# Kernel tuning notes

Hardware: AMD Instinct MI355X
Metric: run time of the kernel (lower is better)

## Reference

```python
import jax, jax.numpy as jnp
import numpy as np

B, T, C = 16, 1023, 2048
N_LAYER, LAYER_ID = 24, 12


def setup_inputs() -> dict:
    key = jax.random.key(0)
    k0, k1, k2, k3, k4 = jax.random.split(key, 5)
    x = jax.random.normal(k0, (B, T, C), jnp.float32)
    # decay schedule exactly as in RWKV_TimeMix.__init__ (first_sa_layer_id = 1)
    f1 = 3.0 + (LAYER_ID - 1) / (N_LAYER - 2) * (1.2 - 3.0)
    f2 = 0.65 + (LAYER_ID - 1) / (N_LAYER - 2) * (0.4 - 0.65)
    h = np.arange(C, dtype=np.float64)
    decay_speed = np.power(f2, h / (C - 1) * 7) * f1
    time_decay = jnp.asarray(np.log(decay_speed), jnp.float32)          # [C]
    time_first = jnp.full((C,), float(np.log(0.3)), jnp.float32)        # [C]
    time_mix = jnp.concatenate([jnp.zeros((C // 2,), jnp.float32),
                                jnp.ones((C - C // 2,), jnp.float32)])  # [C]
    s = 0.02
    Wk = jax.random.normal(k1, (C, C), jnp.float32) * s
    Wv = jax.random.normal(k2, (C, C), jnp.float32) * s
    Wr = jax.random.normal(k3, (C, C), jnp.float32) * s
    Wo = jax.random.normal(k4, (C, C), jnp.float32) * s
    z = jnp.zeros((B, C), jnp.float32)
    return {"x": x, "time_decay": time_decay, "time_first": time_first,
            "time_mix": time_mix, "Wk": Wk, "Wv": Wv, "Wr": Wr, "Wo": Wo,
            "xx": z, "aa": z, "bb": z, "mm": z}


def reference(x, time_decay, time_first, time_mix, Wk, Wv, Wr, Wo, xx, aa, bb, mm):
    Bn, Tn, Cn = x.shape
    # time_shift: prepend carried last-token state xx, drop last
    x_shift = jnp.concatenate([xx[:, None, :], x[:, :-1, :]], axis=1)
    xm = x * time_mix + x_shift * (1.0 - time_mix)
    k = xm @ Wk.T                       # [B, T, C]
    v = xm @ Wv.T
    r = xm @ Wr.T
    # running-max renorm to the nearest power of two: ldexp(0.5, frexp(max_t k).exponent)
    kmax = jax.lax.stop_gradient(jnp.max(k, axis=1))   # [B, C], max over time
    _, expo = jnp.frexp(kmax)
    mm_new = jnp.ldexp(jnp.float32(0.5), expo)          # [B, C]
    k = jnp.exp(k - mm_new[:, None, :])
    kv = k * v
    # TimeX kernel weights: w[c, T-1-delta] = exp(-exp(time_decay[c]) * (delta-1)) = d**(delta-1),
    # w[c, T-1] = exp(time_first[c]); so wk[t] = e_first*k[t] + sum_{u<t} d^{t-1-u} k[u] -> linear scan
    d = jnp.exp(-jnp.exp(time_decay))                   # [C] per-channel decay (= w[...,-3])
    e_first = jnp.exp(time_first)                       # [C] (w[...,-1])
    rsf = jnp.exp(mm - mm_new)                          # rescale carried state to new renorm
    k_seq = jnp.concatenate([(bb * rsf)[:, None, :], k], axis=1)    # [B, T+1, C]
    kv_seq = jnp.concatenate([(aa * rsf)[:, None, :], kv], axis=1)  # [B, T+1, C]

    def step(carry, inp):
        Sk, Skv = carry
        kt, kvt = inp
        out = (e_first * kt + Sk, e_first * kvt + Skv)
        return (d * Sk + kt, d * Skv + kvt), out

    init = (jnp.zeros((Bn, Cn), x.dtype), jnp.zeros((Bn, Cn), x.dtype))
    seq = (jnp.swapaxes(k_seq, 0, 1), jnp.swapaxes(kv_seq, 0, 1))   # [T+1, B, C]
    _, (wk_s, wkv_s) = jax.lax.scan(step, init, seq)
    wk = jnp.swapaxes(wk_s[1:], 0, 1)     # drop state slot -> [B, T, C]
    wkv = jnp.swapaxes(wkv_s[1:], 0, 1)
    rwkv = jax.nn.sigmoid(r) * jnp.nan_to_num(wkv / wk)
    return rwkv @ Wo.T
```

## Files before the change

### kernel.cpp

```cpp
#include <hip/hip_runtime.h>
#include <hip/hip_bf16.h>
#include <math.h>
#include <float.h>

#define BB 16
#define TT 1023
#define CC 2048
#define M_ROWS (BB * TT)
#define MP 16384
#define N3 (3 * CC)
#define NCH 16
#define CHL 64

typedef __attribute__((ext_vector_type(8))) short bfrag;
typedef __attribute__((ext_vector_type(4))) float f32x4;
typedef __attribute__((ext_vector_type(4))) short short4v;

__device__ __forceinline__ void async16(const void* g, void* l) {
  __builtin_amdgcn_global_load_lds((const __attribute__((address_space(1))) void*)g,
                                   (__attribute__((address_space(3))) void*)l, 16, 0, 0);
}

__device__ __forceinline__ short bfb(float f) {
  __hip_bfloat16 h = __float2bfloat16(f);
  return *reinterpret_cast<short*>(&h);
}

__global__ void cast_weights(const float* __restrict__ Wk, const float* __restrict__ Wv,
                             const float* __restrict__ Wr, const float* __restrict__ Wo,
                             __hip_bfloat16* __restrict__ W3, __hip_bfloat16* __restrict__ WoB) {
  size_t i4 = (size_t)blockIdx.x * 256 + threadIdx.x;
  size_t i = i4 * 4;
  float4 a = *(const float4*)(Wk + i);
  float4 b = *(const float4*)(Wv + i);
  float4 c = *(const float4*)(Wr + i);
  float4 d = *(const float4*)(Wo + i);
  *(short4v*)((short*)W3 + i)              = short4v{bfb(a.x), bfb(a.y), bfb(a.z), bfb(a.w)};
  *(short4v*)((short*)W3 + i + CC * CC)    = short4v{bfb(b.x), bfb(b.y), bfb(b.z), bfb(b.w)};
  *(short4v*)((short*)W3 + i + 2 * CC * CC) = short4v{bfb(c.x), bfb(c.y), bfb(c.z), bfb(c.w)};
  *(short4v*)((short*)WoB + i)             = short4v{bfb(d.x), bfb(d.y), bfb(d.z), bfb(d.w)};
}

__global__ void build_xm(const float* __restrict__ x, const float* __restrict__ xx,
                         const float* __restrict__ tmix, __hip_bfloat16* __restrict__ xm) {
  int m = blockIdx.x;
  short* orow = (short*)xm + (size_t)m * CC;
  if (m >= M_ROWS) {
    for (int c = threadIdx.x; c < CC / 4; c += 256)
      ((short4v*)orow)[c] = short4v{0, 0, 0, 0};
    return;
  }
  int b = m / TT, t = m - b * TT;
  const float* xrow = x + (size_t)m * CC;
  const float* xprev = (t == 0) ? (xx + (size_t)b * CC) : (xrow - CC);
  for (int c = threadIdx.x; c < CC / 4; c += 256) {
    float4 xv = ((const float4*)xrow)[c];
    float4 pv = ((const float4*)xprev)[c];
    float4 tm = ((const float4*)tmix)[c];
    ((short4v*)orow)[c] = short4v{
        bfb(xv.x * tm.x + pv.x * (1.0f - tm.x)),
        bfb(xv.y * tm.y + pv.y * (1.0f - tm.y)),
        bfb(xv.z * tm.z + pv.z * (1.0f - tm.z)),
        bfb(xv.w * tm.w + pv.w * (1.0f - tm.w))};
  }
}

template <int MODE>
__global__ __launch_bounds__(512, 2)
void gemm256(const short* __restrict__ A, const short* __restrict__ Bw,
             float* __restrict__ outF, __hip_bfloat16* __restrict__ outV,
             __hip_bfloat16* __restrict__ outR) {
  __shared__ short lds[65536];

  const int lane = threadIdx.x & 63, wid = threadIdx.x >> 6;
  const int wr = wid >> 2, wc = wid & 3;

  const int nx = gridDim.x;
  const int nwg = nx * gridDim.y;
  const int bid = blockIdx.y * nx + blockIdx.x;
  const int q = nwg >> 3;
  const int swz = (bid & 7) * q + (bid >> 3);
  const int mBase = (swz / nx) * 256;
  const int nBase = (swz % nx) * 256;

  const int srow = lane >> 2;
  const int scol = (((lane & 3) ^ ((lane >> 3) & 3)) * 8);
  const int stgOff = wid * 1024 + lane * 8;
  const short* aSrcBase = A  + (size_t)(mBase + wid * 32 + srow) * CC + scol;
  const short* bSrcBase = Bw + (size_t)(nBase + wid * 32 + srow) * CC + scol;

  const int ldOff = (lane & 15) * 32 + (((lane >> 4) ^ ((lane >> 1) & 3)) * 8);

  f32x4 acc[2][4][4] = {};
  bfrag bq[2][4];

#define RGNA(buf, kh) ((buf) * 32768 + (kh) * 8192)
#define RGNB(buf, kh) (16384 + (buf) * 32768 + (kh) * 8192)

#define STG_A(buf, kh, tk) do { \
    const short* _s = aSrcBase + ((tk) * 64 + (kh) * 32); \
    short* _d = lds + RGNA(buf, kh) + stgOff; \
    async16(_s, _d); async16(_s + (size_t)16 * CC, _d + 512); } while (0)

#define STG_B(buf, kh, tk) do { \
    const short* _s = bSrcBase + ((tk) * 64 + (kh) * 32); \
    short* _d = lds + RGNB(buf, kh) + stgOff; \
    async16(_s, _d); async16(_s + (size_t)16 * CC, _d + 512); } while (0)

#define STG4(buf, tk) do { \
    STG_A(buf, 0, tk); STG_B(buf, 0, tk); \
    STG_A(buf, 1, tk); STG_B(buf, 1, tk); } while (0)

#define VM0 asm volatile("s_waitcnt vmcnt(0)" ::: "memory")

#define PHA(buf, STAGE) do { \
    bfrag aq[2][4]; \
    _Pragma("unroll") \
    for (int kh = 0; kh < 2; ++kh) { \
      _Pragma("unroll") \
      for (int n = 0; n < 4; ++n) \
        bq[kh][n] = *(const bfrag*)(lds + RGNB(buf, kh) + (wc * 64 + n * 16) * 32 + ldOff); \
      _Pragma("unroll") \
      for (int f = 0; f < 4; ++f) \
        aq[kh][f] = *(const bfrag*)(lds + RGNA(buf, kh) + (wr * 128 + f * 16) * 32 + ldOff); \
    } \
    STAGE; \
    __builtin_amdgcn_s_barrier(); \
    __builtin_amdgcn_s_setprio(1); \
    _Pragma("unroll") \
    for (int kh = 0; kh < 2; ++kh) \
      _Pragma("unroll") \
      for (int f = 0; f < 4; ++f) \
        _Pragma("unroll") \
        for (int n = 0; n < 4; ++n) \
          acc[0][f][n] = __builtin_amdgcn_mfma_f32_16x16x32_bf16(aq[kh][f], bq[kh][n], acc[0][f][n], 0, 0, 0); \
    __builtin_amdgcn_s_setprio(0); \
    __builtin_amdgcn_s_barrier(); } while (0)

#define PHB(buf, WAIT) do { \
    bfrag aq[2][4]; \
    _Pragma("unroll") \
    for (int kh = 0; kh < 2; ++kh) \
      _Pragma("unroll") \
      for (int f = 0; f < 4; ++f) \
        aq[kh][f] = *(const bfrag*)(lds + RGNA(buf, kh) + (wr * 128 + 64 + f * 16) * 32 + ldOff); \
    __builtin_amdgcn_s_barrier(); \
    __builtin_amdgcn_s_setprio(1); \
    _Pragma("unroll") \
    for (int kh = 0; kh < 2; ++kh) \
      _Pragma("unroll") \
      for (int f = 0; f < 4; ++f) \
        _Pragma("unroll") \
        for (int n = 0; n < 4; ++n) \
          acc[1][f][n] = __builtin_amdgcn_mfma_f32_16x16x32_bf16(aq[kh][f], bq[kh][n], acc[1][f][n], 0, 0, 0); \
    __builtin_amdgcn_s_setprio(0); \
    WAIT; \
    __builtin_amdgcn_s_barrier(); } while (0)

  STG4(0, 0);
  VM0;
  __builtin_amdgcn_s_barrier();

  for (int ti = 0; ti < 30; ti += 2) {
    PHA(0, STG4(1, ti + 1));
    PHB(0, VM0);
    PHA(1, STG4(0, ti + 2));
    PHB(1, VM0);
  }
  PHA(0, STG4(1, 31));
  PHB(0, VM0);
  PHA(1, );
  PHB(1, );

#undef PHA
#undef PHB
#undef VM0
#undef STG4
#undef STG_A
#undef STG_B
#undef RGNA
#undef RGNB

#pragma unroll
  for (int mh = 0; mh < 2; ++mh)
#pragma unroll
    for (int f = 0; f < 4; ++f) {
      const int row0 = mBase + wr * 128 + mh * 64 + f * 16 + (lane >> 4) * 4;
      const int col0 = nBase + wc * 64 + (lane & 15);
#pragma unroll
      for (int n = 0; n < 4; ++n) {
        const int col = col0 + n * 16;
#pragma unroll
        for (int rr = 0; rr < 4; ++rr) {
          const int row = row0 + rr;
          if (row < M_ROWS) {
            float val = acc[mh][f][n][rr];
            if constexpr (MODE == 0) {
              outF[(size_t)row * CC + col] = val;
            } else {
              if (col < CC)          outF[(size_t)row * CC + col] = val;
              else if (col < 2 * CC) outV[(size_t)row * CC + (col - CC)] = __float2bfloat16(val);
              else                   outR[(size_t)row * CC + (col - 2 * CC)] = __float2bfloat16(val);
            }
          }
        }
      }
    }
}

__global__ __launch_bounds__(1024)
void scan_fuse2(const float* __restrict__ kraw, const __hip_bfloat16* __restrict__ v,
                const __hip_bfloat16* __restrict__ r, const float* __restrict__ aa,
                const float* __restrict__ bb, const float* __restrict__ mm,
                const float* __restrict__ tdec, const float* __restrict__ tfir,
                __hip_bfloat16* __restrict__ rwkv) {
  __shared__ float sBk[NCH][64], sBkv[NCH][64], sSk[NCH][64], sSkv[NCH][64];

  const int lane = threadIdx.x & 63, wid = threadIdx.x >> 6;
  const int c = blockIdx.x * 64 + lane;
  const int b = blockIdx.y;
  const int i = b * CC + c;

  const float dexp = expf(tdec[c]);
  const float d    = expf(-dexp);
  const float ef   = expf(tfir[c]);

  const int t0 = wid * CHL;
  const int t1 = (t0 + CHL < TT) ? t0 + CHL : TT;
  const size_t base = (size_t)b * TT * CC + c;

  if (wid < NCH - 1) {
    float Bk = 0.0f, Bkv = 0.0f;
    size_t off = base + (size_t)t0 * CC;
#pragma unroll 4
    for (int t = t0; t < t1; ++t, off += CC) {
      float kk = expf(kraw[off]);
      float kv = kk * __bfloat162float(v[off]);
      Bk = d * Bk + kk;
      Bkv = d * Bkv + kv;
    }
    sBk[wid][lane] = Bk;
    sBkv[wid][lane] = Bkv;
  }
  __syncthreads();

  if (wid == 0) {
    const float d64 = expf(-dexp * (float)CHL);
    const float sc = expf(mm[i]);
    float S = bb[i] * sc, Sv = aa[i] * sc;
#pragma unroll
    for (int j = 0; j < NCH; ++j) {
      sSk[j][lane] = S;
      sSkv[j][lane] = Sv;
      if (j < NCH - 1) {
        S = d64 * S + sBk[j][lane];
        Sv = d64 * Sv + sBkv[j][lane];
      }
    }
  }
  __syncthreads();

  float S = sSk[wid][lane], Sv = sSkv[wid][lane];
  size_t off = base + (size_t)t0 * CC;
#pragma unroll 4
  for (int t = t0; t < t1; ++t, off += CC) {
    float kk = expf(kraw[off]);
    float vv = __bfloat162float(v[off]);
    float rv = __bfloat162float(r[off]);
    float kv = kk * vv;
    float wk = ef * kk + S;
    float wkv = ef * kv + Sv;
    S = d * S + kk;
    Sv = d * Sv + kv;
    float ratio = wkv / wk;
    if (isnan(ratio)) ratio = 0.0f;
    else if (isinf(ratio)) ratio = ratio > 0.0f ? FLT_MAX : -FLT_MAX;
    float sig = 1.0f / (1.0f + expf(-rv));
    rwkv[off] = __float2bfloat16(sig * ratio);
  }
}

extern "C" void kernel_launch(void* const* d_in, const int* in_sizes, int n_in,
                              void* d_out, int out_size, void* d_ws, size_t ws_size,
                              hipStream_t stream) {
  const float* x    = (const float*)d_in[0];
  const float* tdec = (const float*)d_in[1];
  const float* tfir = (const float*)d_in[2];
  const float* tmix = (const float*)d_in[3];
  const float* Wk   = (const float*)d_in[4];
  const float* Wv   = (const float*)d_in[5];
  const float* Wr   = (const float*)d_in[6];
  const float* Wo   = (const float*)d_in[7];
  const float* xx   = (const float*)d_in[8];
  const float* aa   = (const float*)d_in[9];
  const float* bb   = (const float*)d_in[10];
  const float* mm   = (const float*)d_in[11];

  char* ws = (char*)d_ws;
  size_t o = 0;
  __hip_bfloat16* W3  = (__hip_bfloat16*)(ws + o); o += (size_t)N3 * CC * 2;
  __hip_bfloat16* WoB = (__hip_bfloat16*)(ws + o); o += (size_t)CC * CC * 2;
  __hip_bfloat16* xmB = (__hip_bfloat16*)(ws + o); o += (size_t)MP * CC * 2;
  __hip_bfloat16* vB  = (__hip_bfloat16*)(ws + o); o += (size_t)MP * CC * 2;
  __hip_bfloat16* rB  = (__hip_bfloat16*)(ws + o); o += (size_t)MP * CC * 2;

  float* kraw = (float*)d_out;
  __hip_bfloat16* rwkvB = xmB;

  cast_weights<<<CC * CC / 1024, 256, 0, stream>>>(Wk, Wv, Wr, Wo, W3, WoB);
  build_xm<<<MP, 256, 0, stream>>>(x, xx, tmix, xmB);
  gemm256<1><<<dim3(N3 / 256, MP / 256), 512, 0, stream>>>(
      (const short*)xmB, (const short*)W3, kraw, vB, rB);
  scan_fuse2<<<dim3(CC / 64, BB), 1024, 0, stream>>>(kraw, vB, rB, aa, bb, mm,
                                                     tdec, tfir, rwkvB);
  gemm256<0><<<dim3(CC / 256, MP / 256), 512, 0, stream>>>(
      (const short*)rwkvB, (const short*)WoB, (float*)d_out, nullptr, nullptr);
}
```

Before: 787.1 us.

## Restructure GEMM tile loop into interleaved loads/MFMAs and vectorize scan to two channels

The GEMM main loop is reorganised so that each k-tile loads B and A fragments in smaller groups and interleaves them with MFMA batches. It now uses one barrier per tile instead of four, which should cut synchronisation overhead and overlap LDS reads with matrix math. The scan kernel now handles two adjacent channels per thread with float2 and ushort2 vector loads, halving the grid and widening memory accesses. This trades smaller per-phase register sets for fewer barriers, and accepts fewer scan workgroups, which may lower occupancy and latency hiding.

```diff
diff --git a/kernel.cpp b/kernel.cpp
--- a/kernel.cpp
+++ b/kernel.cpp
@@ -24,6 +24,10 @@
 __device__ __forceinline__ short bfb(float f) {
   __hip_bfloat16 h = __float2bfloat16(f);
   return *reinterpret_cast<short*>(&h);
+}
+
+__device__ __forceinline__ float b2f(unsigned short u) {
+  return __uint_as_float((unsigned int)u << 16);
 }
 
 __global__ void cast_weights(const float* __restrict__ Wk, const float* __restrict__ Wv,
@@ -92,7 +96,6 @@
   const int ldOff = (lane & 15) * 32 + (((lane >> 4) ^ ((lane >> 1) & 3)) * 8);
 
   f32x4 acc[2][4][4] = {};
-  bfrag bq[2][4];
 
 #define RGNA(buf, kh) ((buf) * 32768 + (kh) * 8192)
 #define RGNB(buf, kh) (16384 + (buf) * 32768 + (kh) * 8192)
@@ -113,48 +116,37 @@
 
 #define VM0 asm volatile("s_waitcnt vmcnt(0)" ::: "memory")
 
-#define PHA(buf, STAGE) do { \
-    bfrag aq[2][4]; \
+#define LDB(dst, buf, kh) \
     _Pragma("unroll") \
-    for (int kh = 0; kh < 2; ++kh) { \
+    for (int n = 0; n < 4; ++n) \
+      dst[n] = *(const bfrag*)(lds + RGNB(buf, kh) + (wc * 64 + n * 16) * 32 + ldOff);
+
+#define LDA(dst, buf, kh, mh) \
+    _Pragma("unroll") \
+    for (int f = 0; f < 4; ++f) \
+      dst[f] = *(const bfrag*)(lds + RGNA(buf, kh) + (wr * 128 + (mh) * 64 + f * 16) * 32 + ldOff);
+
+#define MM(ai, bi, m) \
+    __builtin_amdgcn_s_setprio(1); \
+    _Pragma("unroll") \
+    for (int f = 0; f < 4; ++f) \
       _Pragma("unroll") \
       for (int n = 0; n < 4; ++n) \
-        bq[kh][n] = *(const bfrag*)(lds + RGNB(buf, kh) + (wc * 64 + n * 16) * 32 + ldOff); \
-      _Pragma("unroll") \
-      for (int f = 0; f < 4; ++f) \
-        aq[kh][f] = *(const bfrag*)(lds + RGNA(buf, kh) + (wr * 128 + f * 16) * 32 + ldOff); \
-    } \
+        acc[m][f][n] = __builtin_amdgcn_mfma_f32_16x16x32_bf16(ai[f], bi[n], acc[m][f][n], 0, 0, 0); \
+    __builtin_amdgcn_s_setprio(0);
+
+#define TILE(buf, STAGE) do { \
+    bfrag a0[4], a1[4], b0[4], b1[4]; \
+    LDB(b0, buf, 0) LDA(a0, buf, 0, 0) \
     STAGE; \
-    __builtin_amdgcn_s_barrier(); \
-    __builtin_amdgcn_s_setprio(1); \
-    _Pragma("unroll") \
-    for (int kh = 0; kh < 2; ++kh) \
-      _Pragma("unroll") \
-      for (int f = 0; f < 4; ++f) \
-        _Pragma("unroll") \
-        for (int n = 0; n < 4; ++n) \
-          acc[0][f][n] = __builtin_amdgcn_mfma_f32_16x16x32_bf16(aq[kh][f], bq[kh][n], acc[0][f][n], 0, 0, 0); \
-    __builtin_amdgcn_s_setprio(0); \
-    __builtin_amdgcn_s_barrier(); } while (0)
-
-#define PHB(buf, WAIT) do { \
-    bfrag aq[2][4]; \
-    _Pragma("unroll") \
-    for (int kh = 0; kh < 2; ++kh) \
-      _Pragma("unroll") \
-      for (int f = 0; f < 4; ++f) \
-        aq[kh][f] = *(const bfrag*)(lds + RGNA(buf, kh) + (wr * 128 + 64 + f * 16) * 32 + ldOff); \
-    __builtin_amdgcn_s_barrier(); \
-    __builtin_amdgcn_s_setprio(1); \
-    _Pragma("unroll") \
-    for (int kh = 0; kh < 2; ++kh) \
-      _Pragma("unroll") \
-      for (int f = 0; f < 4; ++f) \
-        _Pragma("unroll") \
-        for (int n = 0; n < 4; ++n) \
-          acc[1][f][n] = __builtin_amdgcn_mfma_f32_16x16x32_bf16(aq[kh][f], bq[kh][n], acc[1][f][n], 0, 0, 0); \
-    __builtin_amdgcn_s_setprio(0); \
-    WAIT; \
+    MM(a0, b0, 0) \
+    LDA(a1, buf, 0, 1) \
+    MM(a1, b0, 1) \
+    LDB(b1, buf, 1) LDA(a0, buf, 1, 0) \
+    MM(a0, b1, 0) \
+    LDA(a1, buf, 1, 1) \
+    MM(a1, b1, 1) \
+    VM0; \
     __builtin_amdgcn_s_barrier(); } while (0)
 
   STG4(0, 0);
@@ -162,18 +154,26 @@
   __builtin_amdgcn_s_barrier();
 
   for (int ti = 0; ti < 30; ti += 2) {
-    PHA(0, STG4(1, ti + 1));
-    PHB(0, VM0);
-    PHA(1, STG4(0, ti + 2));
-    PHB(1, VM0);
-  }
-  PHA(0, STG4(1, 31));
-  PHB(0, VM0);
-  PHA(1, );
-  PHB(1, );
-
-#undef PHA
-#undef PHB
+    TILE(0, STG4(1, ti + 1));
+    TILE(1, STG4(0, ti + 2));
+  }
+  TILE(0, STG4(1, 31));
+  {
+    bfrag a0[4], a1[4], b0[4], b1[4];
+    LDB(b0, 1, 0) LDA(a0, 1, 0, 0)
+    MM(a0, b0, 0)
+    LDA(a1, 1, 0, 1)
+    MM(a1, b0, 1)
+    LDB(b1, 1, 1) LDA(a0, 1, 1, 0)
+    MM(a0, b1, 0)
+    LDA(a1, 1, 1, 1)
+    MM(a1, b1, 1)
+  }
+
+#undef TILE
+#undef MM
+#undef LDA
+#undef LDB
 #undef VM0
 #undef STG4
 #undef STG_A
@@ -214,30 +214,33 @@
                 const float* __restrict__ bb, const float* __restrict__ mm,
                 const float* __restrict__ tdec, const float* __restrict__ tfir,
                 __hip_bfloat16* __restrict__ rwkv) {
-  __shared__ float sBk[NCH][64], sBkv[NCH][64], sSk[NCH][64], sSkv[NCH][64];
+  __shared__ float2 sBk[NCH][64], sBkv[NCH][64], sSk[NCH][64], sSkv[NCH][64];
 
   const int lane = threadIdx.x & 63, wid = threadIdx.x >> 6;
-  const int c = blockIdx.x * 64 + lane;
+  const int c = blockIdx.x * 128 + lane * 2;
   const int b = blockIdx.y;
   const int i = b * CC + c;
 
-  const float dexp = expf(tdec[c]);
-  const float d    = expf(-dexp);
-  const float ef   = expf(tfir[c]);
+  float2 de, d, ef;
+  de.x = expf(tdec[c]);     de.y = expf(tdec[c + 1]);
+  d.x  = expf(-de.x);       d.y  = expf(-de.y);
+  ef.x = expf(tfir[c]);     ef.y = expf(tfir[c + 1]);
 
   const int t0 = wid * CHL;
   const int t1 = (t0 + CHL < TT) ? t0 + CHL : TT;
   const size_t base = (size_t)b * TT * CC + c;
 
   if (wid < NCH - 1) {
-    float Bk = 0.0f, Bkv = 0.0f;
+    float2 Bk = {0.0f, 0.0f}, Bkv = {0.0f, 0.0f};
     size_t off = base + (size_t)t0 * CC;
 #pragma unroll 4
     for (int t = t0; t < t1; ++t, off += CC) {
-      float kk = expf(kraw[off]);
-      float kv = kk * __bfloat162float(v[off]);
-      Bk = d * Bk + kk;
-      Bkv = d * Bkv + kv;
+      float2 k2 = *(const float2*)(kraw + off);
+      ushort2 v2 = *(const ushort2*)((const unsigned short*)v + off);
+      float kk0 = expf(k2.x), kk1 = expf(k2.y);
+      Bk.x = d.x * Bk.x + kk0;           Bk.y = d.y * Bk.y + kk1;
+      Bkv.x = d.x * Bkv.x + kk0 * b2f(v2.x);
+      Bkv.y = d.y * Bkv.y + kk1 * b2f(v2.y);
     }
     sBk[wid][lane] = Bk;
     sBkv[wid][lane] = Bkv;
@@ -245,38 +248,48 @@
   __syncthreads();
 
   if (wid == 0) {
-    const float d64 = expf(-dexp * (float)CHL);
-    const float sc = expf(mm[i]);
-    float S = bb[i] * sc, Sv = aa[i] * sc;
+    float2 d64, S, Sv;
+    d64.x = expf(-de.x * (float)CHL);  d64.y = expf(-de.y * (float)CHL);
+    float sc0 = expf(mm[i]), sc1 = expf(mm[i + 1]);
+    S.x = bb[i] * sc0;      S.y = bb[i + 1] * sc1;
+    Sv.x = aa[i] * sc0;     Sv.y = aa[i + 1] * sc1;
 #pragma unroll
     for (int j = 0; j < NCH; ++j) {
       sSk[j][lane] = S;
       sSkv[j][lane] = Sv;
       if (j < NCH - 1) {
-        S = d64 * S + sBk[j][lane];
-        Sv = d64 * Sv + sBkv[j][lane];
+        float2 Bk = sBk[j][lane], Bkv = sBkv[j][lane];
+        S.x = d64.x * S.x + Bk.x;    S.y = d64.y * S.y + Bk.y;
+        Sv.x = d64.x * Sv.x + Bkv.x; Sv.y = d64.y * Sv.y + Bkv.y;
       }
     }
   }
   __syncthreads();
 
-  float S = sSk[wid][lane], Sv = sSkv[wid][lane];
+  float2 S = sSk[wid][lane], Sv = sSkv[wid][lane];
   size_t off = base + (size_t)t0 * CC;
 #pragma unroll 4
   for (int t = t0; t < t1; ++t, off += CC) {
-    float kk = expf(kraw[off]);
-    float vv = __bfloat162float(v[off]);
-    float rv = __bfloat162float(r[off]);
-    float kv = kk * vv;
-    float wk = ef * kk + S;
-    float wkv = ef * kv + Sv;
-    S = d * S + kk;
-    Sv = d * Sv + kv;
-    float ratio = wkv / wk;
-    if (isnan(ratio)) ratio = 0.0f;
-    else if (isinf(ratio)) ratio = ratio > 0.0f ? FLT_MAX : -FLT_MAX;
-    float sig = 1.0f / (1.0f + expf(-rv));
-    rwkv[off] = __float2bfloat16(sig * ratio);
+    float2 k2 = *(const float2*)(kraw + off);
+    ushort2 v2 = *(const ushort2*)((const unsigned short*)v + off);
+    ushort2 r2 = *(const ushort2*)((const unsigned short*)r + off);
+    float kk0 = expf(k2.x), kk1 = expf(k2.y);
+    float kv0 = kk0 * b2f(v2.x), kv1 = kk1 * b2f(v2.y);
+    float wk0 = ef.x * kk0 + S.x,   wk1 = ef.y * kk1 + S.y;
+    float wkv0 = ef.x * kv0 + Sv.x, wkv1 = ef.y * kv1 + Sv.y;
+    S.x = d.x * S.x + kk0;   S.y = d.y * S.y + kk1;
+    Sv.x = d.x * Sv.x + kv0; Sv.y = d.y * Sv.y + kv1;
+    float ra0 = wkv0 / wk0, ra1 = wkv1 / wk1;
+    if (isnan(ra0)) ra0 = 0.0f;
+    else if (isinf(ra0)) ra0 = ra0 > 0.0f ? FLT_MAX : -FLT_MAX;
+    if (isnan(ra1)) ra1 = 0.0f;
+    else if (isinf(ra1)) ra1 = ra1 > 0.0f ? FLT_MAX : -FLT_MAX;
+    float s0 = 1.0f / (1.0f + expf(-b2f(r2.x)));
+    float s1 = 1.0f / (1.0f + expf(-b2f(r2.y)));
+    ushort2 o;
+    o.x = (unsigned short)bfb(s0 * ra0);
+    o.y = (unsigned short)bfb(s1 * ra1);
+    *(ushort2*)((unsigned short*)rwkv + off) = o;
   }
 }
 
@@ -311,8 +324,8 @@
   build_xm<<<MP, 256, 0, stream>>>(x, xx, tmix, xmB);
   gemm256<1><<<dim3(N3 / 256, MP / 256), 512, 0, stream>>>(
       (const short*)xmB, (const short*)W3, kraw, vB, rB);
-  scan_fuse2<<<dim3(CC / 64, BB), 1024, 0, stream>>>(kraw, vB, rB, aa, bb, mm,
-                                                     tdec, tfir, rwkvB);
+  scan_fuse2<<<dim3(CC / 128, BB), 1024, 0, stream>>>(kraw, vB, rB, aa, bb, mm,
+                                                      tdec, tfir, rwkvB);
   gemm256<0><<<dim3(CC / 256, MP / 256), 512, 0, stream>>>(
       (const short*)rwkvB, (const short*)WoB, (float*)d_out, nullptr, nullptr);
 }
```

Result: faster. 767.6 us (-2.5%).
